# Kernel tuning notes

Hardware: AMD Instinct MI355X
Metric: run time of the kernel (lower is better)

## Reference

```python
import jax, jax.numpy as jnp
import numpy as np

T, B, V, E, H, L = 70, 64, 10000, 512, 1024, 2


def setup_inputs() -> dict:
    key = jax.random.key(0)
    ks = jax.random.split(key, 10)
    k = float(1.0 / np.sqrt(H))
    u = lambda kk, shape, a: jax.random.uniform(kk, shape, jnp.float32, -a, a)
    return {
        "inputs": jax.random.randint(ks[0], (T, B), 0, V, dtype=jnp.int32),
        "hidden": jnp.zeros((L, B, H), jnp.float32),
        "emb_W": u(ks[1], (V, E), 0.1),
        "Wx0": u(ks[2], (H, E), k),   # nn.Linear weight is [out, in]
        "Wx1": u(ks[3], (H, H), k),
        "Wh0": u(ks[4], (H, H), k),
        "bh0": u(ks[5], (H,), k),
        "Wh1": u(ks[6], (H, H), k),
        "bh1": u(ks[7], (H,), k),
        "Wy": u(ks[8], (V, H), 0.1),
        "by": jnp.zeros((V,), jnp.float32),
    }


def reference(inputs, hidden, emb_W, Wx0, Wx1, Wh0, bh0, Wh1, bh1, Wy, by):
    # Stacked Elman RNN, dropout identity (dp_keep_prob=1.0).
    embedded = emb_W[inputs]  # [T, B, E]

    def step(h, x_t):
        # h: [L, B, H]; x_t: [B, E]
        h0 = jnp.tanh(x_t @ Wx0.T + h[0] @ Wh0.T + bh0)
        h1 = jnp.tanh(h0 @ Wx1.T + h[1] @ Wh1.T + bh1)
        new_h = jnp.stack([h0, h1])  # [L, B, H]
        logits_t = h1 @ Wy.T + by    # [B, V]
        return new_h, logits_t

    h_final, logits = jax.lax.scan(step, hidden, embedded)
    return logits, h_final  # [T, B, V], [L, B, H]
```

## Files before the change

kernel.cpp:

```cpp
#include <hip/hip_runtime.h>
#include <hip/hip_bf16.h>
#include <cmath>
#include <cstdint>


using u16 = unsigned short;
using u32 = unsigned int;
typedef __attribute__((ext_vector_type(8))) short short8;
typedef __attribute__((ext_vector_type(4))) float f32x4;

#define MFMA_BF16(a, b, c) __builtin_amdgcn_mfma_f32_16x16x32_bf16((a), (b), (c), 0, 0, 0)

__device__ __forceinline__ u16 bf16_rne(float x) {
    u32 u = __float_as_uint(x);
    u32 r = u + 0x7FFFu + ((u >> 16) & 1u);
    return (u16)(r >> 16);
}
__device__ __forceinline__ float bf16_f(u16 h) {
    return __uint_as_float(((u32)h) << 16);
}
__device__ __forceinline__ void split2(float x, u16& hi, u16& lo) {
    hi = bf16_rne(x);
    lo = bf16_rne(x - bf16_f(hi));
}

__device__ __forceinline__ void wait_count(int* f, int target) {
    if (threadIdx.x == 0) {
        while (__hip_atomic_load(f, __ATOMIC_ACQUIRE, __HIP_MEMORY_SCOPE_AGENT) < target)
            __builtin_amdgcn_s_sleep(1);
    }
    __syncthreads();
}
__device__ __forceinline__ void signal_done(int* f) {
    __syncthreads();
    if (threadIdx.x == 0)
        __hip_atomic_fetch_add(f, 1, __ATOMIC_RELEASE, __HIP_MEMORY_SCOPE_AGENT);
}

__global__ __launch_bounds__(256) void split_kernel(
    const float* __restrict__ src, u16* __restrict__ hi, u16* __restrict__ lo, int n4)
{
    int g = blockIdx.x * 256 + threadIdx.x;
    if (g >= n4) return;
    float4 v = *reinterpret_cast<const float4*>(src + (size_t)g * 4);
    u16 h0,h1,h2,h3,l0,l1,l2,l3;
    split2(v.x,h0,l0); split2(v.y,h1,l1); split2(v.z,h2,l2); split2(v.w,h3,l3);
    ushort4 H = {h0,h1,h2,h3}, L = {l0,l1,l2,l3};
    *reinterpret_cast<ushort4*>(hi + (size_t)g * 4) = H;
    *reinterpret_cast<ushort4*>(lo + (size_t)g * 4) = L;
}

__global__ __launch_bounds__(256) void gather_split_kernel(
    const float* __restrict__ emb, const int* __restrict__ idx,
    u16* __restrict__ hi, u16* __restrict__ lo, int n4)
{
    int g = blockIdx.x * 256 + threadIdx.x;
    if (g >= n4) return;
    int m  = g >> 7;
    int c4 = g & 127;
    const float* src = emb + (size_t)idx[m] * 512 + c4 * 4;
    float4 v = *reinterpret_cast<const float4*>(src);
    u16 h0,h1,h2,h3,l0,l1,l2,l3;
    split2(v.x,h0,l0); split2(v.y,h1,l1); split2(v.z,h2,l2); split2(v.w,h3,l3);
    ushort4 H = {h0,h1,h2,h3}, L = {l0,l1,l2,l3};
    size_t o = (size_t)m * 512 + c4 * 4;
    *reinterpret_cast<ushort4*>(hi + o) = H;
    *reinterpret_cast<ushort4*>(lo + o) = L;
}

__global__ __launch_bounds__(256) void gemm_mfma(
    const u16* __restrict__ Ah, const u16* __restrict__ Al,
    const u16* __restrict__ Bh, const u16* __restrict__ Bl,
    const float* __restrict__ bias, float* __restrict__ C,
    int M, int N, int K)
{
    __shared__ u16 sAh[128*32], sAl[128*32], sBh[128*32], sBl[128*32];
    const int tid  = threadIdx.x;
    const int lane = tid & 63;
    const int w    = tid >> 6;
    const int wr   = w >> 1, wc = w & 1;
    const int m0   = blockIdx.y * 128, n0 = blockIdx.x * 128;

    f32x4 acc[4][4];
    #pragma unroll
    for (int i = 0; i < 4; ++i)
        #pragma unroll
        for (int j = 0; j < 4; ++j) acc[i][j] = 0.0f;

    for (int k0 = 0; k0 < K; k0 += 32) {
        #pragma unroll
        for (int r = 0; r < 2; ++r) {
            int s   = r * 256 + tid;
            int row = s >> 2, q = s & 3;
            int gq  = q ^ (row & 3);
            int l16 = row * 32 + q * 8;
            size_t ga = (size_t)(m0 + row) * K + k0 + gq * 8;
            int brow = n0 + row; if (brow >= N) brow = N - 1;
            size_t gb = (size_t)brow * K + k0 + gq * 8;
            *reinterpret_cast<int4*>(sAh + l16) = *reinterpret_cast<const int4*>(Ah + ga);
            *reinterpret_cast<int4*>(sAl + l16) = *reinterpret_cast<const int4*>(Al + ga);
            *reinterpret_cast<int4*>(sBh + l16) = *reinterpret_cast<const int4*>(Bh + gb);
            *reinterpret_cast<int4*>(sBl + l16) = *reinterpret_cast<const int4*>(Bl + gb);
        }
        __syncthreads();

        const int q4 = lane >> 4;
        short8 afh[4], afl[4];
        #pragma unroll
        for (int i = 0; i < 4; ++i) {
            int ra  = wr * 64 + i * 16 + (lane & 15);
            int off = ra * 32 + (q4 ^ (ra & 3)) * 8;
            afh[i] = *reinterpret_cast<const short8*>(sAh + off);
            afl[i] = *reinterpret_cast<const short8*>(sAl + off);
        }
        #pragma unroll
        for (int j = 0; j < 4; ++j) {
            int rb  = wc * 64 + j * 16 + (lane & 15);
            int off = rb * 32 + (q4 ^ (rb & 3)) * 8;
            short8 bfh = *reinterpret_cast<const short8*>(sBh + off);
            short8 bfl = *reinterpret_cast<const short8*>(sBl + off);
            #pragma unroll
            for (int i = 0; i < 4; ++i) {
                acc[i][j] = MFMA_BF16(afh[i], bfh, acc[i][j]);
                acc[i][j] = MFMA_BF16(afh[i], bfl, acc[i][j]);
                acc[i][j] = MFMA_BF16(afl[i], bfh, acc[i][j]);
            }
        }
        __syncthreads();
    }

    #pragma unroll
    for (int j = 0; j < 4; ++j) {
        int n = n0 + wc * 64 + j * 16 + (lane & 15);
        if (n < N) {
            float bv = bias[n];
            #pragma unroll
            for (int i = 0; i < 4; ++i) {
                #pragma unroll
                for (int r = 0; r < 4; ++r) {
                    int m = m0 + wr * 64 + i * 16 + (lane >> 4) * 4 + r;
                    C[(size_t)m * N + n] = acc[i][j][r] + bv;
                }
            }
        }
    }
}

__global__ __launch_bounds__(256, 1) void rnn_persist2(
    const float* __restrict__ A0,
    const u16* __restrict__ hs0h, const u16* __restrict__ hs0l,
    const u16* __restrict__ hs1h, const u16* __restrict__ hs1l,
    u16* __restrict__ H0h, u16* __restrict__ H0l,
    u16* __restrict__ H1h, u16* __restrict__ H1l,
    const u16* __restrict__ Wh0h, const u16* __restrict__ Wh0l,
    const u16* __restrict__ Wx1h, const u16* __restrict__ Wx1l,
    const u16* __restrict__ Wh1h, const u16* __restrict__ Wh1l,
    const float* __restrict__ bh1, int* flags)
{
    __shared__ u16 sW[65536];
    const int tid   = threadIdx.x;
    const int lane  = tid & 63;
    const int w     = tid >> 6;
    const int layer = blockIdx.x >> 6;
    const int n0    = (int)(blockIdx.x & 63) * 16;
    const int m0    = w * 16;
    const int rb    = lane & 15;
    const int q4    = lane >> 4;
    const int arow  = m0 + rb;
    const size_t BH = 65536;

    if (layer == 0) {
        for (int i = 0; i < 16; ++i) {
            int s    = i * 256 + tid;
            int arr  = s >> 11;
            int r    = (s >> 7) & 15;
            int g    = s & 127;
            int slot = g ^ (r & 7);
            const u16* src = (arr ? Wh0l : Wh0h) + (size_t)(n0 + r) * 1024 + g * 8;
            *reinterpret_cast<int4*>(sW + arr * 16384 + r * 1024 + slot * 8) =
                *reinterpret_cast<const int4*>(src);
        }
    } else {
        for (int i = 0; i < 32; ++i) {
            int s    = i * 256 + tid;
            int arr  = s >> 12;
            int r    = (s >> 8) & 15;
            int g    = s & 255;
            int slot = g ^ (r & 7);
            const u16* src;
            if (g < 128) src = (arr ? Wx1l : Wx1h) + (size_t)(n0 + r) * 1024 + g * 8;
            else         src = (arr ? Wh1l : Wh1h) + (size_t)(n0 + r) * 1024 + (g - 128) * 8;
            *reinterpret_cast<int4*>(sW + arr * 32768 + r * 2048 + slot * 8) =
                *reinterpret_cast<const int4*>(src);
        }
    }
    __syncthreads();

    if (layer == 0) {
        for (int t = 0; t < 70; ++t) {
            if (t > 0) wait_count(flags + (t - 1), 64);
            const u16* hph = t ? H0h + (size_t)(t - 1) * BH : hs0h;
            const u16* hpl = t ? H0l + (size_t)(t - 1) * BH : hs0l;
            f32x4 acc = {0.f, 0.f, 0.f, 0.f};
            #pragma unroll 8
            for (int kt = 0; kt < 32; ++kt) {
                short8 ah = *reinterpret_cast<const short8*>(hph + (size_t)arow * 1024 + kt * 32 + q4 * 8);
                short8 al = *reinterpret_cast<const short8*>(hpl + (size_t)arow * 1024 + kt * 32 + q4 * 8);
                int slot = (kt * 4 + q4) ^ (rb & 7);
                short8 bh = *reinterpret_cast<const short8*>(sW + rb * 1024 + slot * 8);
                short8 bl = *reinterpret_cast<const short8*>(sW + 16384 + rb * 1024 + slot * 8);
                acc = MFMA_BF16(ah, bh, acc);
                acc = MFMA_BF16(ah, bl, acc);
                acc = MFMA_BF16(al, bh, acc);
            }
            const int n = n0 + rb;
            #pragma unroll
            for (int r = 0; r < 4; ++r) {
                int m = m0 + q4 * 4 + r;
                size_t o = (size_t)t * BH + (size_t)m * 1024 + n;
                float hv = tanhf(acc[r] + A0[o]);
                u16 hi, lo; split2(hv, hi, lo);
                H0h[o] = hi; H0l[o] = lo;
            }
            signal_done(flags + t);
        }
    } else {
        for (int t = 0; t < 70; ++t) {
            wait_count(flags + t, 64);
            if (t > 0) wait_count(flags + 70 + (t - 1), 64);
            const u16* h0h  = H0h + (size_t)t * BH;
            const u16* h0l  = H0l + (size_t)t * BH;
            const u16* h1ph = t ? H1h + (size_t)(t - 1) * BH : hs1h;
            const u16* h1pl = t ? H1l + (size_t)(t - 1) * BH : hs1l;
            f32x4 acc = {0.f, 0.f, 0.f, 0.f};
            #pragma unroll 8
            for (int kt = 0; kt < 32; ++kt) {
                short8 ah = *reinterpret_cast<const short8*>(h0h + (size_t)arow * 1024 + kt * 32 + q4 * 8);
                short8 al = *reinterpret_cast<const short8*>(h0l + (size_t)arow * 1024 + kt * 32 + q4 * 8);
                int slot = (kt * 4 + q4) ^ (rb & 7);
                short8 bh = *reinterpret_cast<const short8*>(sW + rb * 2048 + slot * 8);
                short8 bl = *reinterpret_cast<const short8*>(sW + 32768 + rb * 2048 + slot * 8);
                acc = MFMA_BF16(ah, bh, acc);
                acc = MFMA_BF16(ah, bl, acc);
                acc = MFMA_BF16(al, bh, acc);
            }
            #pragma unroll 8
            for (int kt = 32; kt < 64; ++kt) {
                int ko = (kt - 32) * 32;
                short8 ah = *reinterpret_cast<const short8*>(h1ph + (size_t)arow * 1024 + ko + q4 * 8);
                short8 al = *reinterpret_cast<const short8*>(h1pl + (size_t)arow * 1024 + ko + q4 * 8);
                int slot = (kt * 4 + q4) ^ (rb & 7);
                short8 bh = *reinterpret_cast<const short8*>(sW + rb * 2048 + slot * 8);
                short8 bl = *reinterpret_cast<const short8*>(sW + 32768 + rb * 2048 + slot * 8);
                acc = MFMA_BF16(ah, bh, acc);
                acc = MFMA_BF16(ah, bl, acc);
                acc = MFMA_BF16(al, bh, acc);
            }
            const int n = n0 + rb;
            #pragma unroll
            for (int r = 0; r < 4; ++r) {
                int m = m0 + q4 * 4 + r;
                size_t o = (size_t)t * BH + (size_t)m * 1024 + n;
                float hv = tanhf(acc[r] + bh1[n]);
                u16 hi, lo; split2(hv, hi, lo);
                H1h[o] = hi; H1l[o] = lo;
            }
            signal_done(flags + 70 + t);
        }
    }
}

__global__ __launch_bounds__(256) void hfinal_kernel(
    const u16* __restrict__ H0h, const u16* __restrict__ H0l,
    const u16* __restrict__ H1h, const u16* __restrict__ H1l,
    float* __restrict__ outp)
{
    int i = blockIdx.x * 256 + threadIdx.x;
    outp[i]         = bf16_f(H0h[i]) + bf16_f(H0l[i]);
    outp[65536 + i] = bf16_f(H1h[i]) + bf16_f(H1l[i]);
}

extern "C" void kernel_launch(void* const* d_in, const int* in_sizes, int n_in,
                              void* d_out, int out_size, void* d_ws, size_t ws_size,
                              hipStream_t stream)
{
    const int*   inputs = (const int*)  d_in[0];
    const float* hidden = (const float*)d_in[1];
    const float* embW   = (const float*)d_in[2];
    const float* Wx0    = (const float*)d_in[3];
    const float* Wx1    = (const float*)d_in[4];
    const float* Wh0    = (const float*)d_in[5];
    const float* bh0    = (const float*)d_in[6];
    const float* Wh1    = (const float*)d_in[7];
    const float* bh1    = (const float*)d_in[8];
    const float* Wy     = (const float*)d_in[9];
    const float* by     = (const float*)d_in[10];
    float* out = (float*)d_out;

    const int T = 70, B = 64, V = 10000, E = 512, H = 1024;
    const int M = T * B;
    const size_t MH = (size_t)M * H;
    const size_t BH = (size_t)B * H;

    char* wsb = (char*)d_ws;
    u16*   Wyh  = (u16*)(wsb);
    u16*   Wyl  = Wyh + (size_t)V * H;
    float* buf0 = (float*)(wsb + 40960000);
    u16*   H0h  = (u16*)(wsb + 59310080);
    u16*   H0l  = H0h + MH;
    u16*   H1h  = H0l + MH;
    u16*   H1l  = H1h + MH;
    u16*   Wx0h = H1l + MH;
    u16*   Wx0l = Wx0h + (size_t)H * E;
    u16*   Wx1h = Wx0l + (size_t)H * E;
    u16*   Wx1l = Wx1h + (size_t)H * H;
    u16*   Wh0h = Wx1l + (size_t)H * H;
    u16*   Wh0l = Wh0h + (size_t)H * H;
    u16*   Wh1h = Wh0l + (size_t)H * H;
    u16*   Wh1l = Wh1h + (size_t)H * H;
    u16*   hs0h = Wh1l + (size_t)H * H;
    u16*   hs0l = hs0h + BH;
    u16*   hs1h = hs0l + BH;
    u16*   hs1l = hs1h + BH;

    u16*   Agh   = (u16*)((char*)d_out + 20971520);
    u16*   Agl   = Agh + (size_t)M * E;
    int*   flags = (int*)((char*)d_out + 104857600);

    dim3 blk(256);

    hipMemsetAsync(flags, 0, 140 * sizeof(int), stream);

    split_kernel<<<dim3((H*E)/1024), blk, 0, stream>>>(Wx0, Wx0h, Wx0l, (H*E)/4);
    split_kernel<<<dim3((H*H)/1024), blk, 0, stream>>>(Wx1, Wx1h, Wx1l, (H*H)/4);
    split_kernel<<<dim3((H*H)/1024), blk, 0, stream>>>(Wh0, Wh0h, Wh0l, (H*H)/4);
    split_kernel<<<dim3((H*H)/1024), blk, 0, stream>>>(Wh1, Wh1h, Wh1l, (H*H)/4);
    split_kernel<<<dim3((V*H)/1024), blk, 0, stream>>>(Wy,  Wyh,  Wyl,  (V*H)/4);
    split_kernel<<<dim3(64), blk, 0, stream>>>(hidden,      hs0h, hs0l, (int)BH/4);
    split_kernel<<<dim3(64), blk, 0, stream>>>(hidden + BH, hs1h, hs1l, (int)BH/4);
    gather_split_kernel<<<dim3((M*E)/1024), blk, 0, stream>>>(embW, inputs, Agh, Agl, (M*E)/4);

    gemm_mfma<<<dim3(H/128, M/128), blk, 0, stream>>>(
        Agh, Agl, Wx0h, Wx0l, bh0, buf0, M, H, E);

    {
        const float* A0p = buf0;
        void* args[] = {
            (void*)&A0p,
            (void*)&hs0h, (void*)&hs0l, (void*)&hs1h, (void*)&hs1l,
            (void*)&H0h,  (void*)&H0l,  (void*)&H1h,  (void*)&H1l,
            (void*)&Wh0h, (void*)&Wh0l, (void*)&Wx1h, (void*)&Wx1l,
            (void*)&Wh1h, (void*)&Wh1l, (void*)&bh1, (void*)&flags
        };
        hipLaunchCooperativeKernel(reinterpret_cast<void*>(rnn_persist2),
                                   dim3(128), blk, args, 0, stream);
    }

    hfinal_kernel<<<dim3(256), blk, 0, stream>>>(
        H0h + (size_t)(T-1) * BH, H0l + (size_t)(T-1) * BH,
        H1h + (size_t)(T-1) * BH, H1l + (size_t)(T-1) * BH,
        out + (size_t)M * V);

    gemm_mfma<<<dim3((V + 127)/128, M/128), blk, 0, stream>>>(
        H1h, H1l, Wyh, Wyl, by, out, M, V, H);
}
```

Baseline: 1.798 ms.

## Relax flag atomics and stage hidden-state writes through LDS as 64-bit stores

Relaxes the acquire/release ordering on the inter-block step flags to relaxed. The recurrent outputs are now staged in shared memory and written as packed 64-bit agent-scope atomic stores instead of scattered 16-bit stores. The aim is to cut fence and cache-writeback overhead on the serial per-timestep critical path and to coalesce the stores. Relaxed ordering gives no guarantee that the plain loads of H0/H1 in other blocks see the new data, so the change risks a memory-ordering race.

After: 1.573 ms. 1.14x faster.

```diff
diff --git a/kernel.cpp b/kernel.cpp
--- a/kernel.cpp
+++ b/kernel.cpp
@@ -6,6 +6,7 @@
 
 using u16 = unsigned short;
 using u32 = unsigned int;
+using u64 = unsigned long long;
 typedef __attribute__((ext_vector_type(8))) short short8;
 typedef __attribute__((ext_vector_type(4))) float f32x4;
 
@@ -23,10 +24,13 @@
     hi = bf16_rne(x);
     lo = bf16_rne(x - bf16_f(hi));
 }
+__device__ __forceinline__ u64 pack4(u16 a, u16 b, u16 c, u16 d) {
+    return (u64)a | ((u64)b << 16) | ((u64)c << 32) | ((u64)d << 48);
+}
 
 __device__ __forceinline__ void wait_count(int* f, int target) {
     if (threadIdx.x == 0) {
-        while (__hip_atomic_load(f, __ATOMIC_ACQUIRE, __HIP_MEMORY_SCOPE_AGENT) < target)
+        while (__hip_atomic_load(f, __ATOMIC_RELAXED, __HIP_MEMORY_SCOPE_AGENT) < target)
             __builtin_amdgcn_s_sleep(1);
     }
     __syncthreads();
@@ -34,7 +38,7 @@
 __device__ __forceinline__ void signal_done(int* f) {
     __syncthreads();
     if (threadIdx.x == 0)
-        __hip_atomic_fetch_add(f, 1, __ATOMIC_RELEASE, __HIP_MEMORY_SCOPE_AGENT);
+        __hip_atomic_fetch_add(f, 1, __ATOMIC_RELAXED, __HIP_MEMORY_SCOPE_AGENT);
 }
 
 __global__ __launch_bounds__(256) void split_kernel(
@@ -158,6 +162,7 @@
     const float* __restrict__ bh1, int* flags)
 {
     __shared__ u16 sW[65536];
+    __shared__ float sStage[64 * 17];
     const int tid   = threadIdx.x;
     const int lane  = tid & 63;
     const int w     = tid >> 6;
@@ -168,6 +173,8 @@
     const int q4    = lane >> 4;
     const int arow  = m0 + rb;
     const size_t BH = 65536;
+    const int srow  = tid >> 2;
+    const int sc4   = (tid & 3) * 4;
 
     if (layer == 0) {
         for (int i = 0; i < 16; ++i) {
@@ -218,9 +225,21 @@
             for (int r = 0; r < 4; ++r) {
                 int m = m0 + q4 * 4 + r;
                 size_t o = (size_t)t * BH + (size_t)m * 1024 + n;
-                float hv = tanhf(acc[r] + A0[o]);
-                u16 hi, lo; split2(hv, hi, lo);
-                H0h[o] = hi; H0l[o] = lo;
+                sStage[m * 17 + rb] = tanhf(acc[r] + A0[o]);
+            }
+            __syncthreads();
+            {
+                float f0 = sStage[srow * 17 + sc4 + 0];
+                float f1 = sStage[srow * 17 + sc4 + 1];
+                float f2 = sStage[srow * 17 + sc4 + 2];
+                float f3 = sStage[srow * 17 + sc4 + 3];
+                u16 a,b,c,d, la,lb,lc,ld;
+                split2(f0,a,la); split2(f1,b,lb); split2(f2,c,lc); split2(f3,d,ld);
+                size_t o64 = ((size_t)t * BH + (size_t)srow * 1024 + n0 + sc4) >> 2;
+                __hip_atomic_store((u64*)H0h + o64, pack4(a,b,c,d),
+                                   __ATOMIC_RELAXED, __HIP_MEMORY_SCOPE_AGENT);
+                __hip_atomic_store((u64*)H0l + o64, pack4(la,lb,lc,ld),
+                                   __ATOMIC_RELAXED, __HIP_MEMORY_SCOPE_AGENT);
             }
             signal_done(flags + t);
         }
@@ -260,10 +279,21 @@
             #pragma unroll
             for (int r = 0; r < 4; ++r) {
                 int m = m0 + q4 * 4 + r;
-                size_t o = (size_t)t * BH + (size_t)m * 1024 + n;
-                float hv = tanhf(acc[r] + bh1[n]);
-                u16 hi, lo; split2(hv, hi, lo);
-                H1h[o] = hi; H1l[o] = lo;
+                sStage[m * 17 + rb] = tanhf(acc[r] + bh1[n]);
+            }
+            __syncthreads();
+            {
+                float f0 = sStage[srow * 17 + sc4 + 0];
+                float f1 = sStage[srow * 17 + sc4 + 1];
+                float f2 = sStage[srow * 17 + sc4 + 2];
+                float f3 = sStage[srow * 17 + sc4 + 3];
+                u16 a,b,c,d, la,lb,lc,ld;
+                split2(f0,a,la); split2(f1,b,lb); split2(f2,c,lc); split2(f3,d,ld);
+                size_t o64 = ((size_t)t * BH + (size_t)srow * 1024 + n0 + sc4) >> 2;
+                __hip_atomic_store((u64*)H1h + o64, pack4(a,b,c,d),
+                                   __ATOMIC_RELAXED, __HIP_MEMORY_SCOPE_AGENT);
+                __hip_atomic_store((u64*)H1l + o64, pack4(la,lb,lc,ld),
+                                   __ATOMIC_RELAXED, __HIP_MEMORY_SCOPE_AGENT);
             }
             signal_done(flags + 70 + t);
         }
```
